# Kernel tuning notes

Hardware: AMD Instinct MI355X
Metric: run time of the kernel (lower is better)

Reference implementation:

```python
import jax, jax.numpy as jnp
import numpy as np

OUT_H = 7
OUT_W = 7
RATIO = 2  # sampling_ratio (static)


def _roi_align(feat, boxes, out_h, out_w, sx, sy, ratio):
    """torchvision-style RoIAlign (aligned=False) on a single image.
    feat: [C,H,W], boxes: [N,4] (x1,y1,x2,y2) in image coords.
    sx, sy: spatial scales (W_feat/W_img, H_feat/H_img). Returns [N,C,out_h,out_w]."""
    C, H, W = feat.shape
    N = boxes.shape[0]
    x1 = boxes[:, 0] * sx
    y1 = boxes[:, 1] * sy
    x2 = boxes[:, 2] * sx
    y2 = boxes[:, 3] * sy
    rw = jnp.maximum(x2 - x1, 1.0)
    rh = jnp.maximum(y2 - y1, 1.0)
    bw = rw / out_w
    bh = rh / out_h
    offs = (jnp.arange(ratio, dtype=feat.dtype) + 0.5) / ratio  # sub-bin sample offsets
    # sample coordinates: [N, out*ratio]
    gy = y1[:, None, None] + (jnp.arange(out_h, dtype=feat.dtype)[None, :, None] + offs[None, None, :]) * bh[:, None, None]
    gx = x1[:, None, None] + (jnp.arange(out_w, dtype=feat.dtype)[None, :, None] + offs[None, None, :]) * bw[:, None, None]
    Y = gy.reshape(N, out_h * ratio)
    X = gx.reshape(N, out_w * ratio)
    vy = (Y >= -1.0) & (Y <= H)
    vx = (X >= -1.0) & (X <= W)
    Yc = jnp.clip(Y, 0.0, H - 1)
    Xc = jnp.clip(X, 0.0, W - 1)
    y0 = jnp.floor(Yc).astype(jnp.int32)
    x0 = jnp.floor(Xc).astype(jnp.int32)
    y1i = jnp.minimum(y0 + 1, H - 1)
    x1i = jnp.minimum(x0 + 1, W - 1)
    ly = Yc - y0.astype(Yc.dtype)
    lx = Xc - x0.astype(Xc.dtype)
    hy = 1.0 - ly
    hx = 1.0 - lx

    def g(yi, xi):  # corner gather -> [C, N, out_h*ratio, out_w*ratio]
        return feat[:, yi[:, :, None], xi[:, None, :]]

    val = (hy[:, :, None] * hx[:, None, :]) * g(y0, x0) \
        + (hy[:, :, None] * lx[:, None, :]) * g(y0, x1i) \
        + (ly[:, :, None] * hx[:, None, :]) * g(y1i, x0) \
        + (ly[:, :, None] * lx[:, None, :]) * g(y1i, x1i)
    valid = vy[:, :, None] & vx[:, None, :]
    val = jnp.where(valid[None], val, 0.0)
    # average over the ratio x ratio sampling grid (always divide by ratio^2)
    val = val.reshape(C, N, out_h, ratio, out_w, ratio).mean(axis=(3, 5))
    return val.transpose(1, 0, 2, 3)


def setup_inputs() -> dict:
    key = jax.random.key(0)
    k0, k1, k2, kb = jax.random.split(key, 4)
    img_h, img_w = 800, 1216
    feat0 = jax.random.normal(k0, (1, 256, 200, 304), dtype=jnp.float32)
    feat1 = jax.random.normal(k1, (1, 256, 100, 152), dtype=jnp.float32)
    feat2 = jax.random.normal(k2, (1, 256, 50, 76), dtype=jnp.float32)
    u = jax.random.uniform(kb, (256, 4), dtype=jnp.float32)
    bx1 = u[:, 0] * (img_w - 32)
    by1 = u[:, 1] * (img_h - 32)
    bw = 16.0 + u[:, 2] * 256.0
    bh = 16.0 + u[:, 3] * 256.0
    bx2 = jnp.minimum(bx1 + bw, float(img_w))
    by2 = jnp.minimum(by1 + bh, float(img_h))
    boxes = jnp.stack([bx1, by1, bx2, by2], axis=1)
    return {"feat0": feat0, "feat1": feat1, "feat2": feat2, "boxes": boxes,
            "img_h": img_h, "img_w": img_w}


def reference(feat0, feat1, feat2, boxes, img_h, img_w):
    _, C, H, W = feat0.shape
    # upsample coarser levels by 2**i, half-pixel bilinear == torch align_corners=False
    ups = [feat0]
    for i, f in enumerate([feat1, feat2], 1):
        s = 2 ** i
        ups.append(jax.image.resize(
            f, (f.shape[0], f.shape[1], f.shape[2] * s, f.shape[3] * s), method='bilinear'))
    fused = jnp.concatenate(ups, axis=1)[0]  # [3C, H, W] (single image)
    sx = W / img_w
    sy = H / img_h
    return _roi_align(fused, boxes, OUT_H, OUT_W, sx, sy, RATIO)
```

## Files before the change

kernel.cpp:

```cpp
#include <hip/hip_runtime.h>
#include <hip/hip_fp16.h>

#define H0 200
#define W0 304
#define H1 100
#define W1 152
#define H2 50
#define W2 76
#define CPL 256
#define CTOT 768
#define OH 7
#define OW 7
#define NPOS 49
#define CBLK 128
#define SROWP 131

#define P0 (H0*W0)
#define P1 (H1*W1)
#define P2 (H2*W2)
#define T0_OFF ((size_t)0)
#define T1_OFF ((size_t)P0*CPL)
#define T2_OFF ((size_t)P0*CPL + (size_t)P1*CPL)
#define WS_ELEMS ((size_t)P0*CPL + (size_t)P1*CPL + (size_t)P2*CPL)
#define WS_BYTES (WS_ELEMS * 2)

__device__ __forceinline__ float hat01(float d) {
    return fmaxf(0.0f, 1.0f - fabsf(d));
}

__device__ __forceinline__ unsigned short f2h_rne(float x) {
    return __half_as_ushort(__float2half_rn(x));
}

__global__ void __launch_bounds__(256)
transpose_all_kernel(const float* __restrict__ f0, const float* __restrict__ f1,
                     const float* __restrict__ f2,
                     unsigned short* __restrict__ T0,
                     unsigned short* __restrict__ T1,
                     unsigned short* __restrict__ T2, int n0, int n01) {
    __shared__ unsigned short tile[64][72];
    int b = blockIdx.x;
    const float* in; unsigned short* outp; int P; int rel;
    if (b < n0)       { in = f0; outp = T0; P = P0; rel = b; }
    else if (b < n01) { in = f1; outp = T1; P = P1; rel = b - n0; }
    else              { in = f2; outp = T2; P = P2; rel = b - n01; }
    int p0 = (rel >> 2) * 64;
    int c0 = (rel & 3) * 64;

    int q = threadIdx.x & 15;
    int r = threadIdx.x >> 4;
    bool full = (p0 + 64 <= P);
#pragma unroll
    for (int i = 0; i < 4; ++i) {
        int c = c0 + r + 16 * i;
        int p = p0 + 4 * q;
        float4 v;
        if (full) {
            v = *(const float4*)(in + (size_t)c * P + p);
        } else {
            v.x = (p + 0 < P) ? in[(size_t)c * P + p + 0] : 0.0f;
            v.y = (p + 1 < P) ? in[(size_t)c * P + p + 1] : 0.0f;
            v.z = (p + 2 < P) ? in[(size_t)c * P + p + 2] : 0.0f;
            v.w = (p + 3 < P) ? in[(size_t)c * P + p + 3] : 0.0f;
        }
        tile[4 * q + 0][r + 16 * i] = f2h_rne(v.x);
        tile[4 * q + 1][r + 16 * i] = f2h_rne(v.y);
        tile[4 * q + 2][r + 16 * i] = f2h_rne(v.z);
        tile[4 * q + 3][r + 16 * i] = f2h_rne(v.w);
    }
    __syncthreads();
    int q8 = threadIdx.x & 7;
    int r8 = threadIdx.x >> 3;
#pragma unroll
    for (int i = 0; i < 2; ++i) {
        int p = p0 + r8 + 32 * i;
        if (p < P) {
            uint4 w = *(const uint4*)&tile[r8 + 32 * i][8 * q8];
            *(uint4*)(outp + (size_t)p * CPL + c0 + 8 * q8) = w;
        }
    }
}

template<int TY, int TX, int CH>
__device__ __forceinline__ void tap_loop(const char* __restrict__ Tb,
                                         const int (*__restrict__ s_idx)[6],
                                         const float (*__restrict__ s_w)[6],
                                         float (*__restrict__ sout)[SROWP],
                                         int grp, int col, unsigned laneByte) {
    for (int pos = grp; pos < NPOS; pos += 16) {
        int oh = pos / 7;
        int ow = pos - oh * 7;
        unsigned yb[TY]; float yw[TY];
#pragma unroll
        for (int j = 0; j < TY; ++j) {
            yb[j] = (unsigned)s_idx[oh][j] + laneByte;
            yw[j] = s_w[oh][j];
        }
        unsigned xb[TX]; __half2 xw2[TX];
#pragma unroll
        for (int j = 0; j < TX; ++j) {
            xb[j] = (unsigned)s_idx[7 + ow][j];
            xw2[j] = __float2half2_rn(s_w[7 + ow][j]);
        }
        float a0 = 0.f, a1 = 0.f, a2 = 0.f, a3 = 0.f;
        float a4 = 0.f, a5 = 0.f, a6 = 0.f, a7 = 0.f;
#pragma unroll
        for (int r0 = 0; r0 < TY; r0 += CH) {
            uint4 v[CH][TX];
#pragma unroll
            for (int r = 0; r < CH; ++r) {
                if (r0 + r < TY) {
#pragma unroll
                    for (int b = 0; b < TX; ++b)
                        v[r][b] = *(const uint4*)(Tb + (yb[r0 + r] + xb[b]));
                }
            }
#pragma unroll
            for (int r = 0; r < CH; ++r) {
                if (r0 + r < TY) {
                    __half2 q0 = __float2half2_rn(0.0f);
                    __half2 q1 = q0, q2 = q0, q3 = q0;
#pragma unroll
                    for (int b = 0; b < TX; ++b) {
                        q0 = __hfma2(xw2[b], *(const __half2*)&v[r][b].x, q0);
                        q1 = __hfma2(xw2[b], *(const __half2*)&v[r][b].y, q1);
                        q2 = __hfma2(xw2[b], *(const __half2*)&v[r][b].z, q2);
                        q3 = __hfma2(xw2[b], *(const __half2*)&v[r][b].w, q3);
                    }
                    float wa = yw[r0 + r];
                    a0 = fmaf(wa, __low2float(q0), a0);  a1 = fmaf(wa, __high2float(q0), a1);
                    a2 = fmaf(wa, __low2float(q1), a2);  a3 = fmaf(wa, __high2float(q1), a3);
                    a4 = fmaf(wa, __low2float(q2), a4);  a5 = fmaf(wa, __high2float(q2), a5);
                    a6 = fmaf(wa, __low2float(q3), a6);  a7 = fmaf(wa, __high2float(q3), a7);
                }
            }
        }
        float4 o0, o1;
        o0.x = a0 * 0.25f; o0.y = a1 * 0.25f; o0.z = a2 * 0.25f; o0.w = a3 * 0.25f;
        o1.x = a4 * 0.25f; o1.y = a5 * 0.25f; o1.z = a6 * 0.25f; o1.w = a7 * 0.25f;
        *(float4*)(&sout[pos][col])     = o0;
        *(float4*)(&sout[pos][col + 4]) = o1;
    }
}

__global__ void __launch_bounds__(256, 4)
roi_align_cl6_kernel(const unsigned short* __restrict__ T0p,
                     const unsigned short* __restrict__ T1p,
                     const unsigned short* __restrict__ T2p,
                     const float* __restrict__ boxes,
                     const int* __restrict__ img_h_p,
                     const int* __restrict__ img_w_p,
                     float* __restrict__ out) {
    __shared__ float sout[NPOS][SROWP];
    __shared__ int   s_idx[14][6];
    __shared__ float s_w[14][6];

    const int n = blockIdx.x;
    const int j = blockIdx.y;
    const int lev = j >> 1;
    const int chalf = j & 1;
    const int tid = threadIdx.x;

    const unsigned short* T; int Hc, Wc; float inv_s;
    if (lev == 0)      { T = T0p; Hc = H0; Wc = W0; inv_s = 1.0f;  }
    else if (lev == 1) { T = T1p; Hc = H1; Wc = W1; inv_s = 0.5f;  }
    else               { T = T2p; Hc = H2; Wc = W2; inv_s = 0.25f; }

    if (tid < 14) {
        int axis = (tid >= 7) ? 1 : 0;
        int o = tid - axis * 7;
        float sx = (float)W0 / (float)img_w_p[0];
        float sy = (float)H0 / (float)img_h_p[0];
        float a1v, bs; int Hf, Hca, mul;
        if (axis) {
            a1v = boxes[n * 4 + 0] * sx;
            float a2v = boxes[n * 4 + 2] * sx;
            bs = fmaxf(a2v - a1v, 1.0f) * (1.0f / (float)OW);
            Hf = W0; Hca = Wc; mul = 1;
        } else {
            a1v = boxes[n * 4 + 1] * sy;
            float a2v = boxes[n * 4 + 3] * sy;
            bs = fmaxf(a2v - a1v, 1.0f) * (1.0f / (float)OH);
            Hf = H0; Hca = Hc; mul = Wc;
        }
        int idx[6]; float w[6];
#pragma unroll
        for (int t = 0; t < 6; ++t) { idx[t] = 0; w[t] = 0.0f; }
        if (lev == 0) {
#pragma unroll
            for (int r2 = 0; r2 < 2; ++r2) {
                float Y = a1v + ((float)o + 0.25f + 0.5f * (float)r2) * bs;
                float v = (Y >= -1.0f && Y <= (float)Hf) ? 1.0f : 0.0f;
                float Yc = fminf(fmaxf(Y, 0.0f), (float)(Hf - 1));
                int y0 = (int)Yc; float lf = Yc - (float)y0;
                idx[2 * r2]     = y0;                  w[2 * r2]     = (1.0f - lf) * v;
                idx[2 * r2 + 1] = min(y0 + 1, Hf - 1); w[2 * r2 + 1] = lf * v;
            }
        } else {
            int bases[2]; float w3[2][3];
#pragma unroll
            for (int r2 = 0; r2 < 2; ++r2) {
                float Y = a1v + ((float)o + 0.25f + 0.5f * (float)r2) * bs;
                float v = (Y >= -1.0f && Y <= (float)Hf) ? 1.0f : 0.0f;
                float Yc = fminf(fmaxf(Y, 0.0f), (float)(Hf - 1));
                int y0 = (int)Yc; float lf = Yc - (float)y0; float hf = 1.0f - lf;
                int yf1 = min(y0 + 1, Hf - 1);
                float yc0 = fminf(fmaxf(((float)y0 + 0.5f) * inv_s - 0.5f, 0.0f), (float)(Hca - 1));
                float yc1 = fminf(fmaxf(((float)yf1 + 0.5f) * inv_s - 0.5f, 0.0f), (float)(Hca - 1));
                int b2 = (int)yc0;
                bases[r2] = b2;
#pragma unroll
                for (int t2 = 0; t2 < 3; ++t2) {
                    float j2 = (float)(b2 + t2);
                    w3[r2][t2] = v * (hf * hat01(yc0 - j2) + lf * hat01(yc1 - j2));
                }
            }
            int dmax = (lev == 1) ? 3 : 2;
            int d = min(max(bases[1] - bases[0], 0), dmax);
            w[0] += w3[0][0]; w[1] += w3[0][1]; w[2] += w3[0][2];
            w[d] += w3[1][0]; w[d + 1] += w3[1][1]; w[d + 2] += w3[1][2];
#pragma unroll
            for (int t = 0; t < 6; ++t) idx[t] = min(bases[0] + t, Hca - 1);
        }
#pragma unroll
        for (int t = 0; t < 6; ++t) { s_idx[tid][t] = idx[t] * mul * CPL * 2; s_w[tid][t] = w[t]; }
    }
    __syncthreads();

    const int grp = tid >> 4;
    const int l16 = tid & 15;
    const int col = l16 * 8;
    const unsigned laneByte = (unsigned)(chalf * CBLK + col) * 2u;
    const char* Tb = (const char*)T;

    if (lev == 0)      tap_loop<4, 4, 4>(Tb, s_idx, s_w, sout, grp, col, laneByte);
    else if (lev == 1) tap_loop<6, 6, 3>(Tb, s_idx, s_w, sout, grp, col, laneByte);
    else               tap_loop<5, 5, 3>(Tb, s_idx, s_w, sout, grp, col, laneByte);
    __syncthreads();

    size_t obase = (size_t)n * CTOT * NPOS + (size_t)(lev * CPL + chalf * CBLK) * NPOS;
    int c = tid / NPOS;
    int p = tid - c * NPOS;
    for (int i = tid; i < CBLK * NPOS; i += 256) {
        out[obase + i] = sout[p][c];
        c += 5; p += 11;
        if (p >= NPOS) { p -= NPOS; ++c; }
    }
}

__device__ __forceinline__ void axis_w3_fb(int yf0, int Hf, int Hc, float inv_s,
                                           float lf, int& base, float* w) {
    int yf1 = min(yf0 + 1, Hf - 1);
    float hf = 1.0f - lf;
    float yc0 = fminf(fmaxf(((float)yf0 + 0.5f) * inv_s - 0.5f, 0.0f), (float)(Hc - 1));
    float yc1 = fminf(fmaxf(((float)yf1 + 0.5f) * inv_s - 0.5f, 0.0f), (float)(Hc - 1));
    base = (int)yc0;
#pragma unroll
    for (int r = 0; r < 3; ++r) {
        float j = (float)(base + r);
        w[r] = hf * hat01(yc0 - j) + lf * hat01(yc1 - j);
    }
}

__global__ void __launch_bounds__(256)
roi_align_fused_fb_kernel(const float* __restrict__ f0,
                          const float* __restrict__ f1,
                          const float* __restrict__ f2,
                          const float* __restrict__ boxes,
                          const int* __restrict__ img_h_p,
                          const int* __restrict__ img_w_p,
                          float* __restrict__ out,
                          int total) {
    int i = blockIdx.x * blockDim.x + threadIdx.x;
    if (i >= total) return;
    int ow = i % OW;
    int t = i / OW;
    int oh = t % OH; t /= OH;
    int c = t % CTOT;
    int n = t / CTOT;
    float sx = (float)W0 / (float)img_w_p[0];
    float sy = (float)H0 / (float)img_h_p[0];
    float bx1 = boxes[n * 4 + 0] * sx;
    float by1 = boxes[n * 4 + 1] * sy;
    float bw = fmaxf(boxes[n * 4 + 2] * sx - bx1, 1.0f) / OW;
    float bh = fmaxf(boxes[n * 4 + 3] * sy - by1, 1.0f) / OH;
    int level = c >> 8;
    int cl = c & (CPL - 1);
    const float* f;
    int Hc, Wc; float inv_s;
    if (level == 0)      { f = f0 + (size_t)cl * P0; Hc = H0; Wc = W0; inv_s = 1.0f;  }
    else if (level == 1) { f = f1 + (size_t)cl * P1; Hc = H1; Wc = W1; inv_s = 0.5f;  }
    else                 { f = f2 + (size_t)cl * P2; Hc = H2; Wc = W2; inv_s = 0.25f; }
    float acc = 0.0f;
#pragma unroll
    for (int ry = 0; ry < 2; ++ry) {
        float Y = by1 + ((float)oh + 0.25f + 0.5f * ry) * bh;
        bool vy = (Y >= -1.0f) && (Y <= (float)H0);
        float Yc = fminf(fmaxf(Y, 0.0f), (float)(H0 - 1));
        int y0 = (int)Yc;
        float ly = Yc - (float)y0;
#pragma unroll
        for (int rx = 0; rx < 2; ++rx) {
            float X = bx1 + ((float)ow + 0.25f + 0.5f * rx) * bw;
            bool vx = (X >= -1.0f) && (X <= (float)W0);
            float Xc = fminf(fmaxf(X, 0.0f), (float)(W0 - 1));
            int x0 = (int)Xc;
            float lx = Xc - (float)x0;
            float v;
            if (level == 0) {
                int y1i = min(y0 + 1, H0 - 1), x1i = min(x0 + 1, W0 - 1);
                float hy = 1.0f - ly, hx = 1.0f - lx;
                float v00 = f[y0 * W0 + x0],  v01 = f[y0 * W0 + x1i];
                float v10 = f[y1i * W0 + x0], v11 = f[y1i * W0 + x1i];
                v = hy * (hx * v00 + lx * v01) + ly * (hx * v10 + lx * v11);
            } else {
                int yb, xb; float wy[3], wxl[3];
                axis_w3_fb(y0, H0, Hc, inv_s, ly, yb, wy);
                axis_w3_fb(x0, W0, Wc, inv_s, lx, xb, wxl);
                v = 0.0f;
#pragma unroll
                for (int a = 0; a < 3; ++a) {
                    int row = min(yb + a, Hc - 1) * Wc;
                    float s = 0.0f;
#pragma unroll
                    for (int b = 0; b < 3; ++b)
                        s += wxl[b] * f[row + min(xb + b, Wc - 1)];
                    v += wy[a] * s;
                }
            }
            if (vy && vx) acc += v;
        }
    }
    out[i] = acc * 0.25f;
}

extern "C" void kernel_launch(void* const* d_in, const int* in_sizes, int n_in,
                              void* d_out, int out_size, void* d_ws, size_t ws_size,
                              hipStream_t stream) {
    const float* f0    = (const float*)d_in[0];
    const float* f1    = (const float*)d_in[1];
    const float* f2    = (const float*)d_in[2];
    const float* boxes = (const float*)d_in[3];
    const int* img_h_p = (const int*)d_in[4];
    const int* img_w_p = (const int*)d_in[5];
    float* out = (float*)d_out;
    int N = in_sizes[3] / 4;

    if (ws_size >= WS_BYTES) {
        unsigned short* ws = (unsigned short*)d_ws;
        unsigned short* T0 = ws + T0_OFF;
        unsigned short* T1 = ws + T1_OFF;
        unsigned short* T2 = ws + T2_OFF;
        int n0 = ((P0 + 63) / 64) * 4;
        int n1 = ((P1 + 63) / 64) * 4;
        int n2 = ((P2 + 63) / 64) * 4;
        transpose_all_kernel<<<n0 + n1 + n2, 256, 0, stream>>>(
            f0, f1, f2, T0, T1, T2, n0, n0 + n1);
        roi_align_cl6_kernel<<<dim3(N, 6), 256, 0, stream>>>(
            T0, T1, T2, boxes, img_h_p, img_w_p, out);
    } else {
        int total = N * CTOT * OH * OW;
        roi_align_fused_fb_kernel<<<(total + 255) / 256, 256, 0, stream>>>(
            f0, f1, f2, boxes, img_h_p, img_w_p, out, total);
    }
}
```

Measured before the change: 155.6 us.

## Double-buffer row loads in tap loop, assign contiguous positions, raise occupancy

The tap loop now issues the gather loads for the next tap row into a two-slot register buffer while the current row is accumulated, with sched_barrier fences to keep the loads issued early. This replaces the chunked load-all-then-compute scheme. Each 16-lane group now takes a contiguous run of 3 or 4 output positions instead of a stride-16 walk, and the launch bound is raised from 4 to 5 waves per SIMD to push the register budget down and allow more resident waves. The risks are register spills or pressure at the tighter bound, and slight load imbalance from the last group doing 4 positions.

Result: slower. 159.8 us (+2.7%).

```diff
diff --git a/kernel.cpp b/kernel.cpp
--- a/kernel.cpp
+++ b/kernel.cpp
@@ -81,59 +81,59 @@
     }
 }
 
-template<int TY, int TX, int CH>
+template<int TY, int TX>
 __device__ __forceinline__ void tap_loop(const char* __restrict__ Tb,
                                          const int (*__restrict__ s_idx)[6],
                                          const float (*__restrict__ s_w)[6],
                                          float (*__restrict__ sout)[SROWP],
-                                         int grp, int col, unsigned laneByte) {
-    for (int pos = grp; pos < NPOS; pos += 16) {
-        int oh = pos / 7;
-        int ow = pos - oh * 7;
+                                         int pstart, int pcount, int col,
+                                         unsigned laneByte) {
+    const __half2 hz = __float2half2_rn(0.0f);
+    for (int pi = 0; pi < pcount; ++pi) {
+        const int pos = pstart + pi;
+        const int oh = pos / 7;
+        const int ow = pos - oh * 7;
         unsigned yb[TY]; float yw[TY];
 #pragma unroll
-        for (int j = 0; j < TY; ++j) {
-            yb[j] = (unsigned)s_idx[oh][j] + laneByte;
-            yw[j] = s_w[oh][j];
+        for (int j2 = 0; j2 < TY; ++j2) {
+            yb[j2] = (unsigned)s_idx[oh][j2] + laneByte;
+            yw[j2] = s_w[oh][j2];
         }
         unsigned xb[TX]; __half2 xw2[TX];
 #pragma unroll
-        for (int j = 0; j < TX; ++j) {
-            xb[j] = (unsigned)s_idx[7 + ow][j];
-            xw2[j] = __float2half2_rn(s_w[7 + ow][j]);
+        for (int j2 = 0; j2 < TX; ++j2) {
+            xb[j2] = (unsigned)s_idx[7 + ow][j2];
+            xw2[j2] = __float2half2_rn(s_w[7 + ow][j2]);
         }
         float a0 = 0.f, a1 = 0.f, a2 = 0.f, a3 = 0.f;
         float a4 = 0.f, a5 = 0.f, a6 = 0.f, a7 = 0.f;
-#pragma unroll
-        for (int r0 = 0; r0 < TY; r0 += CH) {
-            uint4 v[CH][TX];
-#pragma unroll
-            for (int r = 0; r < CH; ++r) {
-                if (r0 + r < TY) {
-#pragma unroll
-                    for (int b = 0; b < TX; ++b)
-                        v[r][b] = *(const uint4*)(Tb + (yb[r0 + r] + xb[b]));
-                }
-            }
-#pragma unroll
-            for (int r = 0; r < CH; ++r) {
-                if (r0 + r < TY) {
-                    __half2 q0 = __float2half2_rn(0.0f);
-                    __half2 q1 = q0, q2 = q0, q3 = q0;
-#pragma unroll
-                    for (int b = 0; b < TX; ++b) {
-                        q0 = __hfma2(xw2[b], *(const __half2*)&v[r][b].x, q0);
-                        q1 = __hfma2(xw2[b], *(const __half2*)&v[r][b].y, q1);
-                        q2 = __hfma2(xw2[b], *(const __half2*)&v[r][b].z, q2);
-                        q3 = __hfma2(xw2[b], *(const __half2*)&v[r][b].w, q3);
-                    }
-                    float wa = yw[r0 + r];
-                    a0 = fmaf(wa, __low2float(q0), a0);  a1 = fmaf(wa, __high2float(q0), a1);
-                    a2 = fmaf(wa, __low2float(q1), a2);  a3 = fmaf(wa, __high2float(q1), a3);
-                    a4 = fmaf(wa, __low2float(q2), a4);  a5 = fmaf(wa, __high2float(q2), a5);
-                    a6 = fmaf(wa, __low2float(q3), a6);  a7 = fmaf(wa, __high2float(q3), a7);
-                }
-            }
+        uint4 v[2][TX];
+#pragma unroll
+        for (int b = 0; b < TX; ++b)
+            v[0][b] = *(const uint4*)(Tb + (yb[0] + xb[b]));
+        __builtin_amdgcn_sched_barrier(0);
+#pragma unroll
+        for (int r = 0; r < TY; ++r) {
+            if (r + 1 < TY) {
+#pragma unroll
+                for (int b = 0; b < TX; ++b)
+                    v[(r + 1) & 1][b] = *(const uint4*)(Tb + (yb[r + 1] + xb[b]));
+                __builtin_amdgcn_sched_barrier(0);
+            }
+            __half2 q0 = hz, q1 = hz, q2 = hz, q3 = hz;
+#pragma unroll
+            for (int b = 0; b < TX; ++b) {
+                const __half2 xw = xw2[b];
+                q0 = __hfma2(xw, *(const __half2*)&v[r & 1][b].x, q0);
+                q1 = __hfma2(xw, *(const __half2*)&v[r & 1][b].y, q1);
+                q2 = __hfma2(xw, *(const __half2*)&v[r & 1][b].z, q2);
+                q3 = __hfma2(xw, *(const __half2*)&v[r & 1][b].w, q3);
+            }
+            const float wa = yw[r];
+            a0 = fmaf(wa, __low2float(q0), a0);  a1 = fmaf(wa, __high2float(q0), a1);
+            a2 = fmaf(wa, __low2float(q1), a2);  a3 = fmaf(wa, __high2float(q1), a3);
+            a4 = fmaf(wa, __low2float(q2), a4);  a5 = fmaf(wa, __high2float(q2), a5);
+            a6 = fmaf(wa, __low2float(q3), a6);  a7 = fmaf(wa, __high2float(q3), a7);
         }
         float4 o0, o1;
         o0.x = a0 * 0.25f; o0.y = a1 * 0.25f; o0.z = a2 * 0.25f; o0.w = a3 * 0.25f;
@@ -143,7 +143,7 @@
     }
 }
 
-__global__ void __launch_bounds__(256, 4)
+__global__ void __launch_bounds__(256, 5)
 roi_align_cl6_kernel(const unsigned short* __restrict__ T0p,
                      const unsigned short* __restrict__ T1p,
                      const unsigned short* __restrict__ T2p,
@@ -233,9 +233,12 @@
     const unsigned laneByte = (unsigned)(chalf * CBLK + col) * 2u;
     const char* Tb = (const char*)T;
 
-    if (lev == 0)      tap_loop<4, 4, 4>(Tb, s_idx, s_w, sout, grp, col, laneByte);
-    else if (lev == 1) tap_loop<6, 6, 3>(Tb, s_idx, s_w, sout, grp, col, laneByte);
-    else               tap_loop<5, 5, 3>(Tb, s_idx, s_w, sout, grp, col, laneByte);
+    const int pstart = 3 * grp;
+    const int pcount = (grp == 15) ? 4 : 3;
+
+    if (lev == 0)      tap_loop<4, 4>(Tb, s_idx, s_w, sout, pstart, pcount, col, laneByte);
+    else if (lev == 1) tap_loop<6, 6>(Tb, s_idx, s_w, sout, pstart, pcount, col, laneByte);
+    else               tap_loop<5, 5>(Tb, s_idx, s_w, sout, pstart, pcount, col, laneByte);
     __syncthreads();
 
     size_t obase = (size_t)n * CTOT * NPOS + (size_t)(lev * CPL + chalf * CBLK) * NPOS;
```
